# Kernel tuning notes

Measured on AMD Instinct MI355X. Metric: run time of the kernel, lower is better.

## Reference

```python
import jax, jax.numpy as jnp
import numpy as np

NUM_CLASSES = 80
NUM_TOP_QUERIES = 300
MASK_THRESHOLD = 0.5
OUT_SIZE = 480  # fixed original image size (all orig_target_sizes == 480)


def setup_inputs() -> dict:
    key = jax.random.key(0)
    k1, k2, k3 = jax.random.split(key, 3)
    B, Q, C, Hm, Wm = 2, 300, NUM_CLASSES, 128, 128
    pred_logits = jax.random.normal(k1, (B, Q, C), dtype=jnp.float32)
    pred_boxes = jax.random.uniform(k2, (B, Q, 4), dtype=jnp.float32)  # cxcywh in [0,1]
    pred_masks = jax.random.normal(k3, (B, Q, Hm, Wm), dtype=jnp.float32)
    orig_target_sizes = jnp.ones((B, 2), dtype=jnp.float32) * OUT_SIZE
    return {
        'pred_logits': pred_logits,
        'pred_boxes': pred_boxes,
        'pred_masks': pred_masks,
        'orig_target_sizes': orig_target_sizes,
    }


def _box_cxcywh_to_xyxy(boxes):
    cx, cy, w, h = jnp.split(boxes, 4, axis=-1)
    return jnp.concatenate([cx - 0.5 * w, cy - 0.5 * h, cx + 0.5 * w, cy + 0.5 * h], axis=-1)


def reference(pred_logits, pred_boxes, pred_masks, orig_target_sizes):
    B, Q, C = pred_logits.shape
    Hm, Wm = pred_masks.shape[-2:]
    K = NUM_TOP_QUERIES

    # box conversion + scaling to original image size ([s0,s1,s0,s1] like repeat(1,2))
    scale = jnp.tile(orig_target_sizes, (1, 2))[:, None, :]  # [B,1,4]
    scaled_boxes = _box_cxcywh_to_xyxy(pred_boxes) * scale    # [B,Q,4]

    # focal-loss path: sigmoid scores, flattened top-k over (Q*C)
    scores = jax.nn.sigmoid(pred_logits).reshape(B, Q * C)
    top_scores, top_indices = jax.lax.top_k(scores, K)        # [B,K]
    top_labels = top_indices % C
    query_indices = top_indices // C                          # [B,K]

    selected_boxes = jnp.take_along_axis(scaled_boxes, query_indices[..., None], axis=1)  # [B,K,4]

    # per-sample mask selection + sigmoid + bilinear upsample (align_corners=False)
    sel_masks = jnp.take_along_axis(pred_masks, query_indices[..., None, None], axis=1)   # [B,K,Hm,Wm]
    mask_probs = jax.nn.sigmoid(sel_masks)
    up = jax.vmap(lambda m: jax.image.resize(m, (OUT_SIZE, OUT_SIZE), 'bilinear'))(
        mask_probs.reshape(B * K, Hm, Wm)
    ).reshape(B, K, OUT_SIZE, OUT_SIZE)
    binary_masks = up > MASK_THRESHOLD                        # [B,K,H,W] bool (torch adds channel dim of 1)

    return top_scores, top_labels, selected_boxes, binary_masks
```

## Files before the change

### kernel.cpp

```cpp
#include <hip/hip_runtime.h>
#include <math.h>

#define BATCH 2
#define NQ    300
#define NC    80
#define NFLAT (NQ * NC)
#define TOPK  300
#define HM    128
#define OUTS  480
#define NBKT  4096
#define CAP   4096

#define INVSCALE (128.0 / 480.0)

typedef float v4f __attribute__((ext_vector_type(4)));

__device__ __forceinline__ unsigned mapf(float x) {
    unsigned u = __float_as_uint(x);
    return (u & 0x80000000u) ? ~u : (u | 0x80000000u);
}

__global__ __launch_bounds__(1024) void topk_kernel(
    const float* __restrict__ logits,
    const float* __restrict__ boxes,
    const float* __restrict__ osize,
    float* __restrict__ out,
    int* __restrict__ qidx)
{
    __shared__ unsigned hist[NBKT];
    __shared__ unsigned long long cand[CAP];
    __shared__ unsigned psum[1024];
    __shared__ unsigned sh_T;
    __shared__ unsigned sh_cnt;

    const int b = blockIdx.x;
    const int tid = threadIdx.x;
    const float* lg = logits + (size_t)b * NFLAT;

    for (int i = tid; i < NBKT; i += 1024) hist[i] = 0;
    if (tid == 0) sh_cnt = 0;
    __syncthreads();
    for (int i = tid; i < NFLAT; i += 1024)
        atomicAdd(&hist[mapf(lg[i]) >> 20], 1u);
    __syncthreads();

    unsigned gsum = hist[4 * tid] + hist[4 * tid + 1] + hist[4 * tid + 2] + hist[4 * tid + 3];
    psum[tid] = gsum;
    __syncthreads();
    for (unsigned off = 1; off < 1024; off <<= 1) {
        unsigned v = (tid + off < 1024) ? psum[tid + off] : 0u;
        __syncthreads();
        psum[tid] += v;
        __syncthreads();
    }
    {
        unsigned nxt = (tid == 1023) ? 0u : psum[tid + 1];
        if (psum[tid] >= (unsigned)TOPK && nxt < (unsigned)TOPK) {
            unsigned acc = nxt, T = 4u * (unsigned)tid;
            for (int bk = 4 * tid + 3; bk >= 4 * tid; --bk) {
                if (acc + hist[bk] >= (unsigned)TOPK) { T = (unsigned)bk; break; }
                acc += hist[bk];
            }
            sh_T = T;
        }
    }
    __syncthreads();
    const unsigned T = sh_T;

    for (int i = tid; i < NFLAT; i += 1024) {
        unsigned m = mapf(lg[i]);
        if ((m >> 20) >= T) {
            unsigned pos = atomicAdd(&sh_cnt, 1u);
            if (pos < CAP)
                cand[pos] = ((unsigned long long)m << 32)
                          | (unsigned long long)(0xFFFFFFFFu - (unsigned)i);
        }
    }
    __syncthreads();
    const unsigned cnt = (sh_cnt > CAP) ? CAP : sh_cnt;

    for (unsigned t = tid; t < cnt; t += 1024) {
        const unsigned long long my = cand[t];
        unsigned rank = 0;
        for (unsigned j = 0; j < cnt; ++j) rank += (cand[j] > my) ? 1u : 0u;
        if (rank < (unsigned)TOPK) {
            unsigned idx = 0xFFFFFFFFu - (unsigned)(my & 0xFFFFFFFFull);
            int q = (int)(idx / NC);
            int c = (int)(idx % NC);
            double x = (double)lg[idx];
            double score = 1.0 / (1.0 + exp(-x));

            out[b * TOPK + rank] = (float)score;
            out[BATCH * TOPK + b * TOPK + rank] = (float)c;

            const float* bx = boxes + ((size_t)(b * NQ + q)) * 4;
            double cx = (double)bx[0], cy = (double)bx[1];
            double w  = (double)bx[2], h  = (double)bx[3];
            double s0 = (double)osize[b * 2 + 0];
            double s1 = (double)osize[b * 2 + 1];
            float* ob = out + 2 * BATCH * TOPK + ((size_t)(b * TOPK + rank)) * 4;
            ob[0] = (float)((cx - 0.5 * w) * s0);
            ob[1] = (float)((cy - 0.5 * h) * s1);
            ob[2] = (float)((cx + 0.5 * w) * s0);
            ob[3] = (float)((cy + 0.5 * h) * s1);

            qidx[b * TOPK + rank] = q;
        }
    }
}

#define SLICES   5
#define OROWS    96
#define NUNITS   (BATCH * TOPK * SLICES)
#define MBLOCKS  512

__global__ __launch_bounds__(1024) void mask_kernel(
    const float* __restrict__ masks,
    const int* __restrict__ qidx,
    float* __restrict__ outm)
{
    __shared__ float sig[28 * HM];
    __shared__ int   jt[OUTS];
    __shared__ float ft[OUTS];

    const int tid = threadIdx.x;

    for (int i = tid; i < OUTS; i += 1024) {
        double s = ((double)i + 0.5) * INVSCALE - 0.5;
        int j = (int)floor(s);
        if (j < 0) j = 0;
        if (j > HM - 2) j = HM - 2;
        double f = s - (double)j;
        if (f < 0.0) f = 0.0;
        if (f > 1.0) f = 1.0;
        jt[i] = j;
        ft[i] = (float)f;
    }

    const int yy0 = tid / 120;
    const int qd  = tid % 120;
    const int x0  = qd * 4;
    int   c0 = 0, ar[4];
    float fxr[4];
    #pragma unroll
    for (int j = 0; j < 4; ++j) {
        double sx = ((double)(x0 + j) + 0.5) * INVSCALE - 0.5;
        int jx = (int)floor(sx);
        if (jx < 0) jx = 0;
        if (jx > HM - 2) jx = HM - 2;
        double f = sx - (double)jx;
        if (f < 0.0) f = 0.0;
        if (f > 1.0) f = 1.0;
        if (j == 0) c0 = jx;
        ar[j]  = jx - c0;
        fxr[j] = (float)f;
    }
    const int c1 = c0 + 1;
    const int c2 = (c0 + 2 > HM - 1) ? (HM - 1) : (c0 + 2);
    __syncthreads();

    for (int u = blockIdx.x; u < NUNITS; u += MBLOCKS) {
        const int mask_id = u / SLICES;
        const int slice   = u % SLICES;
        const int b = mask_id / TOPK;
        const int q = qidx[mask_id];
        const int ys = slice * OROWS;
        const int r_lo = jt[ys];
        const int r_hi = jt[ys + OROWS - 1] + 1;
        const int cnt  = r_hi - r_lo + 1;

        __syncthreads();

        const v4f* s4 = (const v4f*)(masks
                          + ((size_t)(b * NQ + q)) * (HM * HM)
                          + (size_t)r_lo * HM);
        const int n4 = cnt * (HM / 4);
        if (tid < n4) {
            v4f v = s4[tid];
            float* dst = sig + tid * 4;
            dst[0] = 1.0f / (1.0f + __expf(-v.x));
            dst[1] = 1.0f / (1.0f + __expf(-v.y));
            dst[2] = 1.0f / (1.0f + __expf(-v.z));
            dst[3] = 1.0f / (1.0f + __expf(-v.w));
        }
        __syncthreads();

        if (tid < 960) {
            float* outp = outm + (size_t)mask_id * (OUTS * OUTS)
                               + (size_t)(ys + yy0) * OUTS + x0;
            #pragma unroll
            for (int it = 0; it < 12; ++it) {
                const int y  = ys + yy0 + it * 8;
                const int jy = jt[y] - r_lo;
                const float wy1 = ft[y];
                const float wy0 = 1.0f - wy1;
                const float* r0 = sig + jy * HM;
                const float* r1 = r0 + HM;

                const float t0 = wy0 * r0[c0] + wy1 * r1[c0];
                const float t1 = wy0 * r0[c1] + wy1 * r1[c1];
                const float t2 = wy0 * r0[c2] + wy1 * r1[c2];

                v4f res;
                #pragma unroll
                for (int j = 0; j < 4; ++j) {
                    const float ta = ar[j] ? t1 : t0;
                    const float tb = ar[j] ? t2 : t1;
                    const float val = ta + fxr[j] * (tb - ta);
                    res[j] = (val > 0.5f) ? 1.0f : 0.0f;
                }
                __builtin_nontemporal_store(res, (v4f*)(outp + (size_t)(it * 8) * OUTS));
            }
        }
    }
}

extern "C" void kernel_launch(void* const* d_in, const int* in_sizes, int n_in,
                              void* d_out, int out_size, void* d_ws, size_t ws_size,
                              hipStream_t stream) {
    const float* logits = (const float*)d_in[0];
    const float* boxes  = (const float*)d_in[1];
    const float* masks  = (const float*)d_in[2];
    const float* osize  = (const float*)d_in[3];
    float* out = (float*)d_out;
    int* qidx = (int*)d_ws;

    topk_kernel<<<BATCH, 1024, 0, stream>>>(logits, boxes, osize, out, qidx);

    mask_kernel<<<MBLOCKS, 1024, 0, stream>>>(masks, qidx, out + 3600);
}
```

Measured before the change: 149.0 us.

## Split mask upsampling into small one-unit-per-block 256-thread blocks

Restructures the mask kernel from 512 persistent 1024-thread blocks looping over 96-row slices into a grid of 18000 blocks of 256 threads, each covering 16 output rows of one mask. Interpolation indices are now computed in float per row instead of through double-precision shared lookup tables, and the nontemporal stores become regular stores. The aim is more blocks resident per CU and less per-iteration synchronisation. In exchange, the smaller tiles re-read overlapping source rows, and float index math could differ slightly from the double version at boundaries.

```diff
diff --git a/kernel.cpp b/kernel.cpp
--- a/kernel.cpp
+++ b/kernel.cpp
@@ -11,7 +11,8 @@
 #define NBKT  4096
 #define CAP   4096
 
-#define INVSCALE (128.0 / 480.0)
+#define INVSCALE  (128.0 / 480.0)
+#define INVSCALEF 0.26666668f
 
 typedef float v4f __attribute__((ext_vector_type(4)));
 
@@ -109,108 +110,97 @@
     }
 }
 
-#define SLICES   5
-#define OROWS    96
-#define NUNITS   (BATCH * TOPK * SLICES)
-#define MBLOCKS  512
-
-__global__ __launch_bounds__(1024) void mask_kernel(
+#define VROWS   16
+#define NVS     (OUTS / VROWS)
+#define MAXR    6
+
+__global__ __launch_bounds__(256) void mask_kernel(
     const float* __restrict__ masks,
     const int* __restrict__ qidx,
     float* __restrict__ outm)
 {
-    __shared__ float sig[28 * HM];
-    __shared__ int   jt[OUTS];
-    __shared__ float ft[OUTS];
+    __shared__ float sig[MAXR * HM];
 
     const int tid = threadIdx.x;
-
-    for (int i = tid; i < OUTS; i += 1024) {
-        double s = ((double)i + 0.5) * INVSCALE - 0.5;
-        int j = (int)floor(s);
-        if (j < 0) j = 0;
-        if (j > HM - 2) j = HM - 2;
-        double f = s - (double)j;
-        if (f < 0.0) f = 0.0;
-        if (f > 1.0) f = 1.0;
-        jt[i] = j;
-        ft[i] = (float)f;
-    }
-
-    const int yy0 = tid / 120;
-    const int qd  = tid % 120;
-    const int x0  = qd * 4;
-    int   c0 = 0, ar[4];
+    const int unit = blockIdx.x;
+    const int mask_id = unit / NVS;
+    const int vs = unit % NVS;
+    const int ys = vs * VROWS;
+    const int b = mask_id / TOPK;
+    const int q = qidx[mask_id];
+
+    float s_first = ((float)ys + 0.5f) * INVSCALEF - 0.5f;
+    float s_last  = ((float)(ys + VROWS - 1) + 0.5f) * INVSCALEF - 0.5f;
+    int r_lo = (int)floorf(s_first);
+    if (r_lo < 0) r_lo = 0; if (r_lo > HM - 2) r_lo = HM - 2;
+    int r_hi = (int)floorf(s_last);
+    if (r_hi < 0) r_hi = 0; if (r_hi > HM - 2) r_hi = HM - 2;
+    r_hi += 1;
+    const int cnt = r_hi - r_lo + 1;
+
+    const v4f* s4 = (const v4f*)(masks
+                      + ((size_t)(b * NQ + q)) * (HM * HM)
+                      + (size_t)r_lo * HM);
+    const int n4 = cnt * (HM / 4);
+    if (tid < n4) {
+        v4f v = s4[tid];
+        float* dst = sig + tid * 4;
+        dst[0] = 1.0f / (1.0f + __expf(-v.x));
+        dst[1] = 1.0f / (1.0f + __expf(-v.y));
+        dst[2] = 1.0f / (1.0f + __expf(-v.z));
+        dst[3] = 1.0f / (1.0f + __expf(-v.w));
+    }
+
+    const int qd = tid % 120;
+    const int yy = tid / 120;
+    const int x0 = qd * 4;
+    int c0 = 0, ar[4];
     float fxr[4];
     #pragma unroll
     for (int j = 0; j < 4; ++j) {
-        double sx = ((double)(x0 + j) + 0.5) * INVSCALE - 0.5;
-        int jx = (int)floor(sx);
-        if (jx < 0) jx = 0;
-        if (jx > HM - 2) jx = HM - 2;
-        double f = sx - (double)jx;
-        if (f < 0.0) f = 0.0;
-        if (f > 1.0) f = 1.0;
+        float sx = ((float)(x0 + j) + 0.5f) * INVSCALEF - 0.5f;
+        int jx = (int)floorf(sx);
+        if (jx < 0) jx = 0; if (jx > HM - 2) jx = HM - 2;
+        float f = sx - (float)jx;
+        f = fminf(fmaxf(f, 0.0f), 1.0f);
         if (j == 0) c0 = jx;
         ar[j]  = jx - c0;
-        fxr[j] = (float)f;
+        fxr[j] = f;
     }
     const int c1 = c0 + 1;
     const int c2 = (c0 + 2 > HM - 1) ? (HM - 1) : (c0 + 2);
-    __syncthreads();
-
-    for (int u = blockIdx.x; u < NUNITS; u += MBLOCKS) {
-        const int mask_id = u / SLICES;
-        const int slice   = u % SLICES;
-        const int b = mask_id / TOPK;
-        const int q = qidx[mask_id];
-        const int ys = slice * OROWS;
-        const int r_lo = jt[ys];
-        const int r_hi = jt[ys + OROWS - 1] + 1;
-        const int cnt  = r_hi - r_lo + 1;
-
-        __syncthreads();
-
-        const v4f* s4 = (const v4f*)(masks
-                          + ((size_t)(b * NQ + q)) * (HM * HM)
-                          + (size_t)r_lo * HM);
-        const int n4 = cnt * (HM / 4);
-        if (tid < n4) {
-            v4f v = s4[tid];
-            float* dst = sig + tid * 4;
-            dst[0] = 1.0f / (1.0f + __expf(-v.x));
-            dst[1] = 1.0f / (1.0f + __expf(-v.y));
-            dst[2] = 1.0f / (1.0f + __expf(-v.z));
-            dst[3] = 1.0f / (1.0f + __expf(-v.w));
-        }
-        __syncthreads();
-
-        if (tid < 960) {
-            float* outp = outm + (size_t)mask_id * (OUTS * OUTS)
-                               + (size_t)(ys + yy0) * OUTS + x0;
+
+    __syncthreads();
+
+    if (tid < 240) {
+        float* outp = outm + (size_t)mask_id * (OUTS * OUTS)
+                           + (size_t)(ys + yy) * OUTS + x0;
+        #pragma unroll
+        for (int it = 0; it < VROWS / 2; ++it) {
+            const int y = ys + yy + it * 2;
+            float sy = ((float)y + 0.5f) * INVSCALEF - 0.5f;
+            int jy = (int)floorf(sy);
+            if (jy < 0) jy = 0; if (jy > HM - 2) jy = HM - 2;
+            float fy = sy - (float)jy;
+            fy = fminf(fmaxf(fy, 0.0f), 1.0f);
+
+            const float* r0 = sig + (size_t)(jy - r_lo) * HM;
+            const float* r1 = r0 + HM;
+            const float wy1 = fy, wy0 = 1.0f - fy;
+
+            const float t0 = wy0 * r0[c0] + wy1 * r1[c0];
+            const float t1 = wy0 * r0[c1] + wy1 * r1[c1];
+            const float t2 = wy0 * r0[c2] + wy1 * r1[c2];
+
+            v4f res;
             #pragma unroll
-            for (int it = 0; it < 12; ++it) {
-                const int y  = ys + yy0 + it * 8;
-                const int jy = jt[y] - r_lo;
-                const float wy1 = ft[y];
-                const float wy0 = 1.0f - wy1;
-                const float* r0 = sig + jy * HM;
-                const float* r1 = r0 + HM;
-
-                const float t0 = wy0 * r0[c0] + wy1 * r1[c0];
-                const float t1 = wy0 * r0[c1] + wy1 * r1[c1];
-                const float t2 = wy0 * r0[c2] + wy1 * r1[c2];
-
-                v4f res;
-                #pragma unroll
-                for (int j = 0; j < 4; ++j) {
-                    const float ta = ar[j] ? t1 : t0;
-                    const float tb = ar[j] ? t2 : t1;
-                    const float val = ta + fxr[j] * (tb - ta);
-                    res[j] = (val > 0.5f) ? 1.0f : 0.0f;
-                }
-                __builtin_nontemporal_store(res, (v4f*)(outp + (size_t)(it * 8) * OUTS));
+            for (int j = 0; j < 4; ++j) {
+                const float ta = ar[j] ? t1 : t0;
+                const float tb = ar[j] ? t2 : t1;
+                const float val = ta + fxr[j] * (tb - ta);
+                res[j] = (val > 0.5f) ? 1.0f : 0.0f;
             }
+            *((v4f*)(outp + (size_t)(it * 2) * OUTS)) = res;
         }
     }
 }
@@ -227,5 +217,5 @@
 
     topk_kernel<<<BATCH, 1024, 0, stream>>>(logits, boxes, osize, out, qidx);
 
-    mask_kernel<<<MBLOCKS, 1024, 0, stream>>>(masks, qidx, out + 3600);
-}
+    mask_kernel<<<BATCH * TOPK * NVS, 256, 0, stream>>>(masks, qidx, out + 3600);
+}
```

Result: no change. 149.9 us (median of 3 runs) (+0.6%).
